# Optimization experiments

Hardware: AMD Instinct MI355X
Metric: run time of the kernel (lower is better)

## Reference

```python
import jax, jax.numpy as jnp
import numpy as np

N_NODES = 50000   # number of graph nodes
N_EDGES = 800000  # avg degree 16
D_IN = 128
D_OUT = 128


def setup_inputs() -> dict:
    key = jax.random.key(0)
    k = jax.random.split(key, 5)
    seq = jax.random.normal(k[0], (N_NODES, D_IN), dtype=jnp.float32)
    # Linear weight, torch layout [out_dim, in_dim], xavier-ish scale
    W = jax.random.normal(k[1], (D_OUT, D_IN), dtype=jnp.float32) * (1.414 / np.sqrt(D_IN))
    b = jnp.zeros((D_OUT,), dtype=jnp.float32)  # bias init fill_(0.0)
    # COO sparse adjacency: out[row] += val * seq_proj[col]
    edge_row = jax.random.randint(k[2], (N_EDGES,), 0, N_NODES, dtype=jnp.int32)
    edge_col = jax.random.randint(k[3], (N_EDGES,), 0, N_NODES, dtype=jnp.int32)
    edge_val = jax.random.uniform(k[4], (N_EDGES,), dtype=jnp.float32)
    return {"seq": seq, "W": W, "b": b,
            "edge_row": edge_row, "edge_col": edge_col, "edge_val": edge_val}


def reference(seq, W, b, edge_row, edge_col, edge_val):
    # seq = self.fc(seq): [N, D_in] @ [D_in, D_out]
    h = seq @ W.T                                   # [N, D_out]
    # out = torch.spmm(adj, h): COO gather-scale-scatter
    msgs = h[edge_col] * edge_val[:, None]          # [E, D_out]
    out = jax.ops.segment_sum(msgs, edge_row, num_segments=N_NODES)  # [N, D_out]
    # bias add + relu (fused epilogue)
    return jax.nn.relu(out + b)
```

## Files before the change

kernel.cpp:

```cpp
#include <hip/hip_runtime.h>

#define NN 50000
#define NE 800000
#define DD 128

#define BK_SHIFT 8
#define NBUCK 196
#define CHUNK 2048
#define NCHUNK 391
#define NGB 782
#define ECAP 8192

#define OFF_H      0
#define OFF_EBIN   3200000
#define OFF_EPACK  6411264
#define OFF_END    9622528
#define OFF_CUR    9672528
#define OFF_WB     9672724
#define WS_FULL_FLOATS 9680916

typedef short short8 __attribute__((ext_vector_type(8)));
typedef float f32x4 __attribute__((ext_vector_type(4)));
typedef unsigned int uint32x2 __attribute__((ext_vector_type(2)));

static __device__ __forceinline__ unsigned int f2bf(float x) {
    unsigned int u = __float_as_uint(x);
    return (u + 0x7fffu + ((u >> 16) & 1u)) >> 16;
}

__global__ __launch_bounds__(256) void k1_scatter_wcast(
        const float* __restrict__ W, unsigned short* __restrict__ Wb,
        const int* __restrict__ erow, const int* __restrict__ ecol,
        const float* __restrict__ eval,
        int* __restrict__ gcur, uint2* __restrict__ ebin) {
    const int t = threadIdx.x;

    if (blockIdx.x < NCHUNK) {
        __shared__ int lh[NBUCK];
        for (int i = t; i < NBUCK; i += 256) lh[i] = 0;
        __syncthreads();
        const int e0 = blockIdx.x * CHUNK;
        for (int i = t; i < CHUNK; i += 256) {
            int e = e0 + i;
            if (e < NE) atomicAdd(&lh[erow[e] >> BK_SHIFT], 1);
        }
        __syncthreads();
        for (int i = t; i < NBUCK; i += 256) {
            int c = lh[i];
            lh[i] = c ? atomicAdd(&gcur[i], c) : 0;
        }
        __syncthreads();
        for (int i = t; i < CHUNK; i += 256) {
            int e = e0 + i;
            if (e < NE) {
                int r = erow[e], c = ecol[e];
                unsigned int vb = __float_as_uint(eval[e]);
                int k = r >> BK_SHIFT;
                int pos = atomicAdd(&lh[k], 1);
                if (pos < ECAP)
                    ebin[(size_t)k * ECAP + pos] =
                        make_uint2(((unsigned)r << 16) | (unsigned)c, vb);
            }
        }
        return;
    }

    const float4* in4 = (const float4*)W;
    uint4* out4 = (uint4*)Wb;
    for (int i = t; i < 2048; i += 256) {
        float4 x = in4[i * 2], y = in4[i * 2 + 1];
        uint4 p;
        p.x = f2bf(x.x) | (f2bf(x.y) << 16);
        p.y = f2bf(x.z) | (f2bf(x.w) << 16);
        p.z = f2bf(y.x) | (f2bf(y.y) << 16);
        p.w = f2bf(y.z) | (f2bf(y.w) << 16);
        out4[i] = p;
    }
}

__global__ __launch_bounds__(256) void k2_fill_gemm(
        const float* __restrict__ seq, const unsigned short* __restrict__ Wb,
        unsigned short* __restrict__ h,
        const uint2* __restrict__ ebin, const int* __restrict__ gcur,
        int* __restrict__ endv, uint2* __restrict__ epack) {
    __shared__ uint4 lds4[3072];
    char* lds = (char*)lds4;
    const int t = threadIdx.x;

    if (blockIdx.x < NBUCK) {
        int* lh = (int*)lds4;
        int* lx = lh + 256;
        const int k = blockIdx.x;
        const size_t s0 = (size_t)k * ECAP;
        int cnt = gcur[k];
        if (cnt > ECAP) cnt = ECAP;
        const size_t s1 = s0 + cnt;
        const int r0 = k << BK_SHIFT;

        lh[t] = 0;
        __syncthreads();
        for (size_t e = s0 + t; e < s1; e += 256)
            atomicAdd(&lh[(ebin[e].x >> 16) & 255], 1);
        __syncthreads();

        const int myc = lh[t];
        lx[t] = myc;
        __syncthreads();
        for (int off = 1; off < 256; off <<= 1) {
            int y = (t >= off) ? lx[t - off] : 0;
            __syncthreads();
            lx[t] += y;
            __syncthreads();
        }
        const int incl = lx[t];
        const int row = r0 + t;
        if (row < NN) endv[row] = (int)s0 + incl;
        __syncthreads();
        lh[t] = (int)s0 + incl - myc;
        __syncthreads();

        for (size_t e = s0 + t; e < s1; e += 256) {
            uint2 ed = ebin[e];
            int pos = atomicAdd(&lh[(ed.x >> 16) & 255], 1);
            epack[pos] = make_uint2(ed.x & 0xffffu, ed.y);
        }
        return;
    }

    const int base = (blockIdx.x - NBUCK) * 64;
#define BS_OFF 16384

    {
        const uint4* wg = (const uint4*)Wb;
        for (int i = t; i < 2048; i += 256) {
            int o = i >> 4, seg = i & 15;
            int byte = o * 256 + seg * 16;
            *(uint4*)(lds + BS_OFF + (byte ^ ((o & 7) << 4))) = wg[i];
        }
    }
    {
        const int row = t >> 2, n = base + row;
        const int c0 = (t & 3) * 4;
        const float4* Sr = (const float4*)(seq + (size_t)n * 128);
        const bool ok = (n < NN);
#pragma unroll
        for (int i = 0; i < 4; ++i) {
            int cc = c0 + i;
            float4 x = ok ? Sr[cc * 2]     : make_float4(0.f, 0.f, 0.f, 0.f);
            float4 y = ok ? Sr[cc * 2 + 1] : make_float4(0.f, 0.f, 0.f, 0.f);
            uint4 p;
            p.x = f2bf(x.x) | (f2bf(x.y) << 16);
            p.y = f2bf(x.z) | (f2bf(x.w) << 16);
            p.z = f2bf(y.x) | (f2bf(y.y) << 16);
            p.w = f2bf(y.z) | (f2bf(y.w) << 16);
            int byte = row * 256 + cc * 16;
            *(uint4*)(lds + (byte ^ ((row & 7) << 4))) = p;
        }
    }
    __syncthreads();

    const int l = t & 63, wv = t >> 6;
    const int lr = l & 15, kg = l >> 4;
    const int arow = wv * 16 + lr;
    f32x4 acc[8] = {};

#pragma unroll
    for (int ks = 0; ks < 4; ++ks) {
        const int kbyte = ks * 64 + kg * 16;
        short8 av = *(short8*)(lds + ((arow * 256 + kbyte) ^ ((arow & 7) << 4)));
#pragma unroll
        for (int c = 0; c < 8; ++c) {
            const int o = c * 16 + lr;
            short8 bv = *(short8*)(lds + BS_OFF +
                                   ((o * 256 + kbyte) ^ ((o & 7) << 4)));
            acc[c] = __builtin_amdgcn_mfma_f32_16x16x32_bf16(av, bv, acc[c], 0, 0, 0);
        }
    }

#pragma unroll
    for (int c = 0; c < 8; ++c) {
#pragma unroll
        for (int r = 0; r < 4; ++r) {
            int n = base + wv * 16 + kg * 4 + r;
            if (n < NN)
                h[(size_t)n * DD + c * 16 + lr] = (unsigned short)f2bf(acc[c][r]);
        }
    }
}

__global__ __launch_bounds__(256) void gather_kernel(const unsigned short* __restrict__ h,
                                                     const int* __restrict__ end,
                                                     const unsigned int* __restrict__ epack,
                                                     const float* __restrict__ b,
                                                     float* __restrict__ out) {
    const int row  = blockIdx.x * 4 + (threadIdx.x >> 6);
    const int lane = threadIdx.x & 63;
    const int slot = lane >> 4;
    const int sub  = lane & 15;
    const int begin = (row & 255) ? end[row - 1] : (row >> BK_SHIFT) * ECAP;
    const int e1 = end[row];

    float acc[8] = {0.f, 0.f, 0.f, 0.f, 0.f, 0.f, 0.f, 0.f};
    const unsigned short* hp = h + sub * 8;

#define BODY(EE) do {                                                          \
        uint32x2 cv = __builtin_nontemporal_load(                              \
            (const uint32x2*)(epack + (size_t)(EE) * 2));                      \
        float v = __uint_as_float(cv.y);                                       \
        uint4 hv = *(const uint4*)(hp + (size_t)cv.x * DD);                    \
        unsigned int uu;                                                       \
        uu = hv.x;                                                             \
        acc[0] = fmaf(v, __uint_as_float(uu << 16),          acc[0]);          \
        acc[1] = fmaf(v, __uint_as_float(uu & 0xffff0000u),  acc[1]);          \
        uu = hv.y;                                                             \
        acc[2] = fmaf(v, __uint_as_float(uu << 16),          acc[2]);          \
        acc[3] = fmaf(v, __uint_as_float(uu & 0xffff0000u),  acc[3]);          \
        uu = hv.z;                                                             \
        acc[4] = fmaf(v, __uint_as_float(uu << 16),          acc[4]);          \
        acc[5] = fmaf(v, __uint_as_float(uu & 0xffff0000u),  acc[5]);          \
        uu = hv.w;                                                             \
        acc[6] = fmaf(v, __uint_as_float(uu << 16),          acc[6]);          \
        acc[7] = fmaf(v, __uint_as_float(uu & 0xffff0000u),  acc[7]);          \
    } while (0)

    int e = begin + slot;
    for (; e + 12 < e1; e += 16) { BODY(e); BODY(e + 4); BODY(e + 8); BODY(e + 12); }
    for (; e < e1; e += 4) BODY(e);
#undef BODY

#pragma unroll
    for (int i = 0; i < 8; ++i) {
        acc[i] += __shfl_xor(acc[i], 16);
        acc[i] += __shfl_xor(acc[i], 32);
    }

    if (slot == 0) {
        const float4* b4 = (const float4*)(b + sub * 8);
        float4 b0 = b4[0], b1 = b4[1];
        f32x4 o0, o1;
        o0.x = fmaxf(acc[0] + b0.x, 0.f);
        o0.y = fmaxf(acc[1] + b0.y, 0.f);
        o0.z = fmaxf(acc[2] + b0.z, 0.f);
        o0.w = fmaxf(acc[3] + b0.w, 0.f);
        o1.x = fmaxf(acc[4] + b1.x, 0.f);
        o1.y = fmaxf(acc[5] + b1.y, 0.f);
        o1.z = fmaxf(acc[6] + b1.z, 0.f);
        o1.w = fmaxf(acc[7] + b1.w, 0.f);
        f32x4* op = (f32x4*)(out + (size_t)row * DD + sub * 8);
        __builtin_nontemporal_store(o0, op);
        __builtin_nontemporal_store(o1, op + 1);
    }
}

extern "C" void kernel_launch(void* const* d_in, const int* in_sizes, int n_in,
                              void* d_out, int out_size, void* d_ws, size_t ws_size,
                              hipStream_t stream) {
    const float* seq  = (const float*)d_in[0];
    const float* W    = (const float*)d_in[1];
    const float* b    = (const float*)d_in[2];
    const int*   erow = (const int*)d_in[3];
    const int*   ecol = (const int*)d_in[4];
    const float* eval = (const float*)d_in[5];
    float* out = (float*)d_out;

    float* wsf = (float*)d_ws;
    unsigned short* h  = (unsigned short*)(wsf + OFF_H);
    uint2* ebin  = (uint2*)(wsf + OFF_EBIN);
    uint2* epack = (uint2*)(wsf + OFF_EPACK);
    int*   endv  = (int*)(wsf + OFF_END);
    int*   gcur  = (int*)(wsf + OFF_CUR);
    unsigned short* Wb = (unsigned short*)(wsf + OFF_WB);

    hipMemsetAsync(gcur, 0, NBUCK * sizeof(int), stream);
    k1_scatter_wcast<<<NCHUNK + 1, 256, 0, stream>>>(W, Wb, erow, ecol, eval,
                                                     gcur, ebin);
    k2_fill_gemm<<<NBUCK + NGB, 256, 0, stream>>>(seq, Wb, h, ebin, gcur,
                                                  endv, epack);
    gather_kernel<<<NN / 4, 256, 0, stream>>>(h, endv, (const unsigned int*)epack,
                                              b, out);
}
```

Measured before the change: 84.70 us.

## Fuse GEMM into scatter kernel, split CSR fill, pack edge value as bf16

Moves the bf16 GEMM blocks into the first kernel alongside the edge bucketing, converting W to bf16 inside each GEMM block instead of in a separate pass. The per-bucket CSR fill becomes its own small kernel. Edge records in epack shrink from 8 to 4 bytes by storing the edge value as bf16 in the upper half, which lowers gather-phase edge traffic. In exchange every GEMM block redoes the W conversion, the 196-block CSR fill runs alone with little parallelism, and edge weights lose precision to bf16.

```diff
diff --git a/kernel.cpp b/kernel.cpp
--- a/kernel.cpp
+++ b/kernel.cpp
@@ -14,29 +14,30 @@
 #define OFF_H      0
 #define OFF_EBIN   3200000
 #define OFF_EPACK  6411264
-#define OFF_END    9622528
-#define OFF_CUR    9672528
-#define OFF_WB     9672724
-#define WS_FULL_FLOATS 9680916
+#define OFF_END    8016896
+#define OFF_CUR    8066896
+#define WS_FULL_FLOATS 8067092
 
 typedef short short8 __attribute__((ext_vector_type(8)));
 typedef float f32x4 __attribute__((ext_vector_type(4)));
-typedef unsigned int uint32x2 __attribute__((ext_vector_type(2)));
 
 static __device__ __forceinline__ unsigned int f2bf(float x) {
     unsigned int u = __float_as_uint(x);
     return (u + 0x7fffu + ((u >> 16) & 1u)) >> 16;
 }
 
-__global__ __launch_bounds__(256) void k1_scatter_wcast(
-        const float* __restrict__ W, unsigned short* __restrict__ Wb,
+__global__ __launch_bounds__(256) void k1_scatter_gemm(
+        const float* __restrict__ seq, const float* __restrict__ W,
+        unsigned short* __restrict__ h,
         const int* __restrict__ erow, const int* __restrict__ ecol,
         const float* __restrict__ eval,
         int* __restrict__ gcur, uint2* __restrict__ ebin) {
+    __shared__ uint4 lds4[3072];
+    char* lds = (char*)lds4;
     const int t = threadIdx.x;
 
     if (blockIdx.x < NCHUNK) {
-        __shared__ int lh[NBUCK];
+        int* lh = (int*)lds4;
         for (int i = t; i < NBUCK; i += 256) lh[i] = 0;
         __syncthreads();
         const int e0 = blockIdx.x * CHUNK;
@@ -65,77 +66,22 @@
         return;
     }
 
-    const float4* in4 = (const float4*)W;
-    uint4* out4 = (uint4*)Wb;
-    for (int i = t; i < 2048; i += 256) {
-        float4 x = in4[i * 2], y = in4[i * 2 + 1];
-        uint4 p;
-        p.x = f2bf(x.x) | (f2bf(x.y) << 16);
-        p.y = f2bf(x.z) | (f2bf(x.w) << 16);
-        p.z = f2bf(y.x) | (f2bf(y.y) << 16);
-        p.w = f2bf(y.z) | (f2bf(y.w) << 16);
-        out4[i] = p;
-    }
-}
-
-__global__ __launch_bounds__(256) void k2_fill_gemm(
-        const float* __restrict__ seq, const unsigned short* __restrict__ Wb,
-        unsigned short* __restrict__ h,
-        const uint2* __restrict__ ebin, const int* __restrict__ gcur,
-        int* __restrict__ endv, uint2* __restrict__ epack) {
-    __shared__ uint4 lds4[3072];
-    char* lds = (char*)lds4;
-    const int t = threadIdx.x;
-
-    if (blockIdx.x < NBUCK) {
-        int* lh = (int*)lds4;
-        int* lx = lh + 256;
-        const int k = blockIdx.x;
-        const size_t s0 = (size_t)k * ECAP;
-        int cnt = gcur[k];
-        if (cnt > ECAP) cnt = ECAP;
-        const size_t s1 = s0 + cnt;
-        const int r0 = k << BK_SHIFT;
-
-        lh[t] = 0;
-        __syncthreads();
-        for (size_t e = s0 + t; e < s1; e += 256)
-            atomicAdd(&lh[(ebin[e].x >> 16) & 255], 1);
-        __syncthreads();
-
-        const int myc = lh[t];
-        lx[t] = myc;
-        __syncthreads();
-        for (int off = 1; off < 256; off <<= 1) {
-            int y = (t >= off) ? lx[t - off] : 0;
-            __syncthreads();
-            lx[t] += y;
-            __syncthreads();
-        }
-        const int incl = lx[t];
-        const int row = r0 + t;
-        if (row < NN) endv[row] = (int)s0 + incl;
-        __syncthreads();
-        lh[t] = (int)s0 + incl - myc;
-        __syncthreads();
-
-        for (size_t e = s0 + t; e < s1; e += 256) {
-            uint2 ed = ebin[e];
-            int pos = atomicAdd(&lh[(ed.x >> 16) & 255], 1);
-            epack[pos] = make_uint2(ed.x & 0xffffu, ed.y);
-        }
-        return;
-    }
-
-    const int base = (blockIdx.x - NBUCK) * 64;
+    const int base = (blockIdx.x - NCHUNK) * 64;
 #define BS_OFF 16384
 
     {
-        const uint4* wg = (const uint4*)Wb;
-        for (int i = t; i < 2048; i += 256) {
-            int o = i >> 4, seg = i & 15;
-            int byte = o * 256 + seg * 16;
-            *(uint4*)(lds + BS_OFF + (byte ^ ((o & 7) << 4))) = wg[i];
+        const int o = t >> 1, ksb = (t & 1) * 64;
+        const float4* Wr = (const float4*)(W + o * 128 + ksb);
+#pragma unroll
+        for (int i = 0; i < 16; i += 2) {
+            float4 x = Wr[i], y = Wr[i + 1];
+            uint4 p;
+            p.x = f2bf(x.x) | (f2bf(x.y) << 16);
+            p.y = f2bf(x.z) | (f2bf(x.w) << 16);
+            p.z = f2bf(y.x) | (f2bf(y.y) << 16);
+            p.w = f2bf(y.z) | (f2bf(y.w) << 16);
+            int byte = o * 256 + (ksb + i * 4) * 2;
+            *(uint4*)(lds + BS_OFF + (byte ^ ((o & 7) << 4))) = p;
         }
     }
     {
@@ -188,6 +134,49 @@
     }
 }
 
+__global__ __launch_bounds__(256) void csr_fill(const uint2* __restrict__ ebin,
+                                                const int* __restrict__ gcur,
+                                                int* __restrict__ endv,
+                                                unsigned int* __restrict__ epack) {
+    __shared__ int lh[256];
+    __shared__ int lx[256];
+    const int k = blockIdx.x;
+    const int t = threadIdx.x;
+    const size_t s0 = (size_t)k * ECAP;
+    int cnt = gcur[k];
+    if (cnt > ECAP) cnt = ECAP;
+    const size_t s1 = s0 + cnt;
+    const int r0 = k << BK_SHIFT;
+
+    lh[t] = 0;
+    __syncthreads();
+    for (size_t e = s0 + t; e < s1; e += 256)
+        atomicAdd(&lh[(ebin[e].x >> 16) & 255], 1);
+    __syncthreads();
+
+    const int myc = lh[t];
+    lx[t] = myc;
+    __syncthreads();
+    for (int off = 1; off < 256; off <<= 1) {
+        int y = (t >= off) ? lx[t - off] : 0;
+        __syncthreads();
+        lx[t] += y;
+        __syncthreads();
+    }
+    const int incl = lx[t];
+    const int row = r0 + t;
+    if (row < NN) endv[row] = (int)s0 + incl;
+    __syncthreads();
+    lh[t] = (int)s0 + incl - myc;
+    __syncthreads();
+
+    for (size_t e = s0 + t; e < s1; e += 256) {
+        uint2 ed = ebin[e];
+        int pos = atomicAdd(&lh[(ed.x >> 16) & 255], 1);
+        epack[pos] = (ed.x & 0xffffu) | (f2bf(__uint_as_float(ed.y)) << 16);
+    }
+}
+
 __global__ __launch_bounds__(256) void gather_kernel(const unsigned short* __restrict__ h,
                                                      const int* __restrict__ end,
                                                      const unsigned int* __restrict__ epack,
@@ -204,10 +193,9 @@
     const unsigned short* hp = h + sub * 8;
 
 #define BODY(EE) do {                                                          \
-        uint32x2 cv = __builtin_nontemporal_load(                              \
-            (const uint32x2*)(epack + (size_t)(EE) * 2));                      \
-        float v = __uint_as_float(cv.y);                                       \
-        uint4 hv = *(const uint4*)(hp + (size_t)cv.x * DD);                    \
+        unsigned int cv = __builtin_nontemporal_load(epack + (EE));            \
+        float v = __uint_as_float(cv & 0xffff0000u);                           \
+        uint4 hv = *(const uint4*)(hp + (size_t)(cv & 0xffffu) * DD);          \
         unsigned int uu;                                                       \
         uu = hv.x;                                                             \
         acc[0] = fmaf(v, __uint_as_float(uu << 16),          acc[0]);          \
@@ -266,16 +254,13 @@
     float* wsf = (float*)d_ws;
     unsigned short* h  = (unsigned short*)(wsf + OFF_H);
     uint2* ebin  = (uint2*)(wsf + OFF_EBIN);
-    uint2* epack = (uint2*)(wsf + OFF_EPACK);
+    unsigned int* epack = (unsigned int*)(wsf + OFF_EPACK);
     int*   endv  = (int*)(wsf + OFF_END);
     int*   gcur  = (int*)(wsf + OFF_CUR);
-    unsigned short* Wb = (unsigned short*)(wsf + OFF_WB);
 
     hipMemsetAsync(gcur, 0, NBUCK * sizeof(int), stream);
-    k1_scatter_wcast<<<NCHUNK + 1, 256, 0, stream>>>(W, Wb, erow, ecol, eval,
-                                                     gcur, ebin);
-    k2_fill_gemm<<<NBUCK + NGB, 256, 0, stream>>>(seq, Wb, h, ebin, gcur,
-                                                  endv, epack);
-    gather_kernel<<<NN / 4, 256, 0, stream>>>(h, endv, (const unsigned int*)epack,
-                                              b, out);
-}
+    k1_scatter_gemm<<<NCHUNK + NGB, 256, 0, stream>>>(seq, W, h, erow, ecol,
+                                                      eval, gcur, ebin);
+    csr_fill<<<NBUCK, 256, 0, stream>>>(ebin, gcur, endv, epack);
+    gather_kernel<<<NN / 4, 256, 0, stream>>>(h, endv, epack, b, out);
+}
```

Measured after the change: 82.91 us. 2.1% less time.
